# Performance work log

Measured on AMD Instinct MI355X. Metric: run time of the kernel, lower is better.

Reference implementation:

```python
import jax, jax.numpy as jnp
import numpy as np

N_STATE = 1024
N_HEAD = 16
D_K = N_STATE // N_HEAD  # 64


def setup_inputs() -> dict:
    key = jax.random.key(0)
    ks = jax.random.split(key, 12)
    B, S = 2, 2048
    s = 1.0 / np.sqrt(N_STATE)
    inp = {
        "q": jax.random.normal(ks[0], (B, S, N_STATE), jnp.float32),
        "k": jax.random.normal(ks[1], (B, S, N_STATE), jnp.float32),
        "v": jax.random.normal(ks[2], (B, S, N_STATE), jnp.float32),
        # Linear weights in torch layout [out_features, in_features]
        "Wq": jax.random.normal(ks[3], (N_STATE, N_STATE), jnp.float32) * s,
        "bq": jax.random.normal(ks[4], (N_STATE,), jnp.float32) * s,
        "Wk": jax.random.normal(ks[5], (N_STATE, N_STATE), jnp.float32) * s,
        "bk": jax.random.normal(ks[6], (N_STATE,), jnp.float32) * s,
        "Wv": jax.random.normal(ks[7], (N_STATE, N_STATE), jnp.float32) * s,
        "bv": jax.random.normal(ks[8], (N_STATE,), jnp.float32) * s,
        "Wo": jax.random.normal(ks[9], (N_STATE, N_STATE), jnp.float32) * s,
        "bo": jax.random.normal(ks[10], (N_STATE,), jnp.float32) * s,
    }
    return inp


def reference(q, k, v, Wq, bq, Wk, bk, Wv, bv, Wo, bo):
    B = q.shape[0]
    # projections (torch Linear: x @ W.T + b), split heads -> [B, H, S, d]
    def proj(x, W, b):
        y = jnp.einsum('bsi,oi->bso', x, W) + b
        return y.reshape(B, -1, N_HEAD, D_K).transpose(0, 2, 1, 3)
    qh = proj(q, Wq, bq)
    kh = proj(k, Wk, bk)
    vh = proj(v, Wv, bv)
    # scaled dot-product attention, full [B,H,Sq,Sk] scores as in original
    scores = jnp.einsum('bhqd,bhkd->bhqk', qh, kh) / np.sqrt(D_K).astype(np.float32)
    attn = jax.nn.softmax(scores, axis=-1)
    out = jnp.einsum('bhqk,bhkd->bhqd', attn, vh)
    out = out.transpose(0, 2, 1, 3).reshape(B, -1, N_HEAD * D_K)
    return jnp.einsum('bsi,oi->bso', out, Wo) + bo
```

## Files before the change

### kernel.cpp

```cpp
#include <hip/hip_runtime.h>
#include <stdint.h>

typedef __attribute__((ext_vector_type(8))) short short8;
typedef __attribute__((ext_vector_type(4))) float f32x4;
typedef __attribute__((ext_vector_type(4))) uint32_t u32x4;

#if __has_builtin(__builtin_amdgcn_exp2f)
#define EXP2(x) __builtin_amdgcn_exp2f(x)
#else
#define EXP2(x) exp2f(x)
#endif

__device__ __forceinline__ short f2bf(float f){
  uint32_t u = __builtin_bit_cast(uint32_t, f);
  return (short)((u + 0x8000u) >> 16);
}
__device__ __forceinline__ float bf2f(short s){
  return __builtin_bit_cast(float, (uint32_t)(uint16_t)s << 16);
}
__device__ __forceinline__ uint32_t pk2(float lo, float hi){
  uint32_t a = __builtin_bit_cast(uint32_t, lo) + 0x8000u;
  uint32_t b = __builtin_bit_cast(uint32_t, hi) + 0x8000u;
#if __has_builtin(__builtin_amdgcn_perm)
  return __builtin_amdgcn_perm(b, a, 0x07060302u);
#else
  return (b & 0xFFFF0000u) | (a >> 16);
#endif
}
__device__ __forceinline__ void gload16(const void* g, void* l){
  __builtin_amdgcn_global_load_lds((const __attribute__((address_space(1))) void*)g,
                                   (__attribute__((address_space(3))) void*)l, 16, 0, 0);
}

__global__ __launch_bounds__(512) void cvt_all(
    const float* __restrict__ q, const float* __restrict__ k, const float* __restrict__ v,
    const float* __restrict__ wq, const float* __restrict__ wk, const float* __restrict__ wv,
    const float* __restrict__ wo, short* __restrict__ dst){
  const size_t SQ = 4096ull*1024ull, NW = 1024ull*1024ull;
  size_t e = (size_t)(blockIdx.x*512u + threadIdx.x)*8ull;
  const float* src; size_t rel;
  if (e < 3*SQ){ size_t which = e / SQ; src = which==0?q:(which==1?k:v); rel = e - which*SQ; }
  else { size_t e2 = e - 3*SQ; size_t which = e2 / NW;
         src = which==0?wq:(which==1?wk:(which==2?wv:wo)); rel = e2 - which*NW; }
  float4 a = *(const float4*)(src + rel);
  float4 b = *(const float4*)(src + rel + 4);
  u32x4 r = { pk2(a.x,a.y), pk2(a.z,a.w), pk2(b.x,b.y), pk2(b.z,b.w) };
  *(u32x4*)(dst + e) = r;
}

template<int MODE, int NWAVE>
__device__ __forceinline__ void gemm_body(const short* __restrict__ A, const short* __restrict__ Bw,
    const float* __restrict__ bias, void* __restrict__ Cout, float scale, int m0, int n0){
  const int K = 1024;
  const int NT  = NWAVE*64;
  const int SW  = 1024/NT;
  const int RPS = NT/8;
  const int NI  = (NWAVE==4) ? 4 : 2;
  const int WCOL = NI*16;
  __shared__ short Al[128*64];
  __shared__ short Bl[128*64];
  int tid = threadIdx.x;
  int w = tid >> 6, lane = tid & 63, lr = lane & 15, lg = lane >> 4;
  int wr = (NWAVE==4) ? (w >> 1) : (w >> 2);
  int wc = (NWAVE==4) ? (w & 1)  : (w & 3);
  f32x4 acc[4][NI] = {};
  int row0 = tid >> 3;
  int qc0  = (tid & 7) ^ (row0 & 7);
  const short* Ag = A  + (size_t)(m0 + row0)*K + qc0*8;
  const short* Bg = Bw + (size_t)(n0 + row0)*K + qc0*8;
  char* Alb = (char*)Al + tid*16;
  char* Blb = (char*)Bl + tid*16;
  int ra[4], rb[NI];
#pragma unroll
  for (int mi=0; mi<4; ++mi) ra[mi] = wr*64 + mi*16 + lr;
#pragma unroll
  for (int ni=0; ni<NI; ++ni) rb[ni] = wc*WCOL + ni*16 + lr;
  for (int k0 = 0; k0 < K; k0 += 64){
#pragma unroll
    for (int s=0; s<SW; ++s) gload16(Ag + k0 + (size_t)(s*RPS)*K, Alb + s*NT*16);
#pragma unroll
    for (int s=0; s<SW; ++s) gload16(Bg + k0 + (size_t)(s*RPS)*K, Blb + s*NT*16);
    __syncthreads();
#pragma unroll
    for (int kk=0; kk<2; ++kk){
      short8 av[4], bv[NI];
#pragma unroll
      for (int mi=0; mi<4; ++mi)
        av[mi] = *(const short8*)((char*)Al + ra[mi]*128 + (((kk*4 + lg) ^ (ra[mi] & 7)) << 4));
#pragma unroll
      for (int ni=0; ni<NI; ++ni)
        bv[ni] = *(const short8*)((char*)Bl + rb[ni]*128 + (((kk*4 + lg) ^ (rb[ni] & 7)) << 4));
#pragma unroll
      for (int mi=0; mi<4; ++mi)
#pragma unroll
        for (int ni=0; ni<NI; ++ni){
          if (MODE == 2)
            acc[mi][ni] = __builtin_amdgcn_mfma_f32_16x16x32_bf16(bv[ni], av[mi], acc[mi][ni], 0, 0, 0);
          else
            acc[mi][ni] = __builtin_amdgcn_mfma_f32_16x16x32_bf16(av[mi], bv[ni], acc[mi][ni], 0, 0, 0);
        }
    }
    __syncthreads();
  }
#pragma unroll
  for (int ni=0; ni<NI; ++ni){
#pragma unroll
    for (int mi=0; mi<4; ++mi){
      if (MODE == 2){
        int srow = m0 + wr*64 + mi*16 + lr;
        int b = srow >> 11, s = srow & 2047;
#pragma unroll
        for (int i2=0; i2<4; ++i2){
          int dcol = n0 + wc*WCOL + ni*16 + lg*4 + i2;
          int h = dcol >> 6, d = dcol & 63;
          float val = acc[mi][ni][i2] + bias[dcol];
          ((short*)Cout)[(((size_t)(b*16 + h))*64 + d)*2048 + s] = f2bf(val);
        }
      } else {
        int col = n0 + wc*WCOL + ni*16 + lr;
        float bb = bias[col];
#pragma unroll
        for (int i2=0; i2<4; ++i2){
          int row = m0 + wr*64 + mi*16 + lg*4 + i2;
          float val = (acc[mi][ni][i2] + bb) * scale;
          if (MODE == 0){
            int b = row >> 11, s = row & 2047, h = col >> 6, d = col & 63;
            ((short*)Cout)[(((size_t)(b*16 + h))*2048 + s)*64 + d] = f2bf(val);
          } else {
            ((float*)Cout)[(size_t)row*1024 + col] = val;
          }
        }
      }
    }
  }
}

__global__ __launch_bounds__(512) void gemm_qkv(
    const short* __restrict__ qb, const short* __restrict__ kb, const short* __restrict__ vb,
    const short* __restrict__ Wqb, const short* __restrict__ Wkb, const short* __restrict__ Wvb,
    const float* __restrict__ bq, const float* __restrict__ bk, const float* __restrict__ bv,
    short* __restrict__ Qh, short* __restrict__ Kh, short* __restrict__ VhT, float qscale){
  int f = blockIdx.y*gridDim.x + blockIdx.x;
  int L = (f & 7)*96 + (f >> 3);
  int z = L >> 8, r = L & 255;
  int m0 = (r >> 3)*128, n0 = (r & 7)*128;
  const short* A  = z==0 ? qb  : (z==1 ? kb  : vb);
  const short* Bw = z==0 ? Wqb : (z==1 ? Wkb : Wvb);
  const float* bi = z==0 ? bq  : (z==1 ? bk  : bv);
  short* C        = z==0 ? Qh  : (z==1 ? Kh  : VhT);
  if (z == 2) gemm_body<2,8>(A, Bw, bi, (void*)C, 1.0f, m0, n0);
  else        gemm_body<0,8>(A, Bw, bi, (void*)C, z==0 ? qscale : 1.0f, m0, n0);
}

__global__ __launch_bounds__(512) void gemm_out(const short* __restrict__ A, const short* __restrict__ Bw,
    const float* __restrict__ bias, float* __restrict__ Cout){
  int f = blockIdx.y*gridDim.x + blockIdx.x;
  int L = (f & 7)*32 + (f >> 3);
  int m0 = (L >> 3)*128, n0 = (L & 7)*128;
  gemm_body<1,8>(A, Bw, bias, (void*)Cout, 1.0f, m0, n0);
}

__global__ __launch_bounds__(512, 4) void attn_fwd(const short* __restrict__ Qh, const short* __restrict__ Kh,
    const short* __restrict__ VhT, short* __restrict__ Op0, short* __restrict__ Op1,
    float* __restrict__ Ls){
  const int S = 2048;
  int i = blockIdx.y*gridDim.x + blockIdx.x;
  int L = (i & 7)*64 + (i >> 3);
  int bh = L >> 4, r4 = L & 15;
  int qt = r4 >> 1, kh = r4 & 1;
  __shared__ short Kl[4][4096];
  __shared__ short Vl[4][4096];
  int tid = threadIdx.x, w = tid >> 6, lane = tid & 63, lr = lane & 15, lg = lane >> 4;
  const short* Qb = Qh  + (size_t)bh*S*64;
  const short* Kb = Kh  + (size_t)bh*S*64 + (size_t)kh*16*4096;
  const short* Vb = VhT + (size_t)bh*64*2048 + (size_t)kh*16*64;
  short* Op = kh ? Op1 : Op0;
  int q0 = qt*256 + w*32;
  short8 aq[2][2];
#pragma unroll
  for (int m=0; m<2; ++m)
#pragma unroll
    for (int h=0; h<2; ++h)
      aq[m][h] = *(const short8*)&Qb[(size_t)(q0 + m*16 + lr)*64 + h*32 + lg*8];
  f32x4 o[2][4] = {};
  f32x4 o1[2] = {};
  short8 ones;
#pragma unroll
  for (int j=0; j<8; ++j) ones[j] = (short)0x3F80;
  int koff = tid*16;
  int kr = tid >> 3, kc = tid & 7;
  int ksw = (kr & 3) | (((kr >> 3) & 1) << 2);
  int ksrc = kr*64 + ((kc ^ ksw) << 3);
  int vsrc = kr*2048 + ((kc ^ (kr & 7)) << 3);
  int Rbase = 8*(lr >> 2) + (lr & 3);
  int sR = (lr & 3) | (((lr >> 2) & 1) << 2);
  int slot0 = (lg ^ sR) << 3, slot1 = ((lg + 4) ^ sR) << 3;
  int vx = lr & 7;
#pragma unroll
  for (int t=0; t<4; ++t){
    gload16(Kb + (size_t)t*4096 + ksrc, (char*)&Kl[t][0] + koff);
    gload16(Vb + vsrc + t*64,           (char*)&Vl[t][0] + koff);
  }
  asm volatile("s_waitcnt vmcnt(4)" ::: "memory");
  __builtin_amdgcn_sched_barrier(0);
  __builtin_amdgcn_s_barrier();

  for (int p = 0; p < 8; ++p){
    __builtin_amdgcn_s_setprio(1);
#pragma unroll
    for (int u = 0; u < 2; ++u){
      int buf = (2*p + u) & 3;
      const short* Kbuf = &Kl[buf][0];
      short8 pa[2][2];
      {
        uint32_t Wp[2][2][2][2];
#pragma unroll
        for (int nf=0; nf<4; ++nf){
          int R = Rbase + (nf & 1)*4 + (nf >> 1)*32;
          short8 ak0 = *(const short8*)&Kbuf[R*64 + slot0];
          short8 ak1 = *(const short8*)&Kbuf[R*64 + slot1];
#pragma unroll
          for (int m=0; m<2; ++m){
            f32x4 z = {};
            z = __builtin_amdgcn_mfma_f32_16x16x32_bf16(ak0, aq[m][0], z, 0, 0, 0);
            z = __builtin_amdgcn_mfma_f32_16x16x32_bf16(ak1, aq[m][1], z, 0, 0, 0);
            float p0 = EXP2(z[0]), p1 = EXP2(z[1]);
            float p2 = EXP2(z[2]), p3 = EXP2(z[3]);
            Wp[m][nf >> 1][nf & 1][0] = pk2(p0, p1);
            Wp[m][nf >> 1][nf & 1][1] = pk2(p2, p3);
          }
        }
#pragma unroll
        for (int m=0; m<2; ++m)
#pragma unroll
          for (int c=0; c<2; ++c){
            union { uint32_t u4[4]; short8 s; } tt;
            tt.u4[0] = Wp[m][c][0][0]; tt.u4[1] = Wp[m][c][0][1];
            tt.u4[2] = Wp[m][c][1][0]; tt.u4[3] = Wp[m][c][1][1];
            pa[m][c] = tt.s;
          }
      }
      const short* Vbuf = &Vl[buf][0];
#pragma unroll
      for (int df=0; df<4; ++df){
        int rowv = (df*16 + lr)*64;
        short8 vb0 = *(const short8*)&Vbuf[rowv + ((lg ^ vx) << 3)];
        short8 vb1 = *(const short8*)&Vbuf[rowv + (((4 + lg) ^ vx) << 3)];
#pragma unroll
        for (int m=0; m<2; ++m){
          o[m][df] = __builtin_amdgcn_mfma_f32_16x16x32_bf16(pa[m][0], vb0, o[m][df], 0, 0, 0);
          o[m][df] = __builtin_amdgcn_mfma_f32_16x16x32_bf16(pa[m][1], vb1, o[m][df], 0, 0, 0);
        }
      }
#pragma unroll
      for (int m=0; m<2; ++m){
        o1[m] = __builtin_amdgcn_mfma_f32_16x16x32_bf16(pa[m][0], ones, o1[m], 0, 0, 0);
        o1[m] = __builtin_amdgcn_mfma_f32_16x16x32_bf16(pa[m][1], ones, o1[m], 0, 0, 0);
      }
    }
    __builtin_amdgcn_s_setprio(0);
    if (p < 7){
      asm volatile("s_waitcnt vmcnt(0)" ::: "memory");
      __builtin_amdgcn_sched_barrier(0);
      __builtin_amdgcn_s_barrier();
      if (p < 6){
#pragma unroll
        for (int u = 0; u < 2; ++u){
          int t = 2*p + 4 + u, nb = t & 3;
          gload16(Kb + (size_t)t*4096 + ksrc, (char*)&Kl[nb][0] + koff);
          gload16(Vb + vsrc + t*64,           (char*)&Vl[nb][0] + koff);
        }
      }
    }
  }
#pragma unroll
  for (int m=0; m<2; ++m){
#pragma unroll
    for (int df=0; df<4; ++df)
#pragma unroll
      for (int i2=0; i2<4; ++i2){
        int row = q0 + m*16 + lg*4 + i2;
        Op[((size_t)(bh*2048 + row))*64 + df*16 + lr] = f2bf(o[m][df][i2]);
      }
    if (lr == 0){
#pragma unroll
      for (int i2=0; i2<4; ++i2){
        int row = q0 + m*16 + lg*4 + i2;
        Ls[kh*65536 + bh*2048 + row] = o1[m][i2];
      }
    }
  }
}

__global__ __launch_bounds__(256) void attn_merge(const short* __restrict__ Op0, const short* __restrict__ Op1,
    const float* __restrict__ Ls, short* __restrict__ AO){
  size_t e = (size_t)(blockIdx.x*256u + threadIdx.x)*8ull;
  int d = (int)(e & 63);
  size_t rowg = e >> 6;
  float rinv = 1.0f / (Ls[rowg] + Ls[65536 + rowg]);
  short8 a = *(const short8*)&Op0[e];
  short8 b8 = *(const short8*)&Op1[e];
  int bh = (int)(rowg >> 11), qq = (int)(rowg & 2047);
  int b = bh >> 4, h = bh & 15;
  short8 r;
#pragma unroll
  for (int j=0; j<8; ++j) r[j] = f2bf((bf2f(a[j]) + bf2f(b8[j])) * rinv);
  *(short8*)&AO[((size_t)(b*2048 + qq))*1024 + h*64 + d] = r;
}

extern "C" void kernel_launch(void* const* d_in, const int* in_sizes, int n_in,
                              void* d_out, int out_size, void* d_ws, size_t ws_size,
                              hipStream_t stream){
  const float* q  = (const float*)d_in[0];
  const float* k  = (const float*)d_in[1];
  const float* v  = (const float*)d_in[2];
  const float* Wq = (const float*)d_in[3];
  const float* bq = (const float*)d_in[4];
  const float* Wk = (const float*)d_in[5];
  const float* bk = (const float*)d_in[6];
  const float* Wv = (const float*)d_in[7];
  const float* bv = (const float*)d_in[8];
  const float* Wo = (const float*)d_in[9];
  const float* bo = (const float*)d_in[10];

  const size_t SQ = 4096ull*1024ull, NW = 1024ull*1024ull;
  short* ws  = (short*)d_ws;
  short* qb  = ws;
  short* kb  = ws + SQ;
  short* vb  = ws + 2*SQ;
  short* Wqb = ws + 3*SQ;
  short* Wkb = Wqb + NW;
  short* Wvb = Wkb + NW;
  short* Wob = Wvb + NW;
  short* Qh  = Wob + NW;
  short* Kh  = Qh + SQ;
  short* VhT = Kh + SQ;
  short* AO  = qb;
  short* Op0 = kb;
  short* Op1 = vb;
  float* Ls  = (float*)Wqb;

  const float Csc = 0.18033688011112042f;

  cvt_all<<<4096, 512, 0, stream>>>(q, k, v, Wq, Wk, Wv, Wo, ws);
  gemm_qkv<<<dim3(16, 48), 512, 0, stream>>>(qb, kb, vb, Wqb, Wkb, Wvb, bq, bk, bv, Qh, Kh, VhT, Csc);
  attn_fwd<<<dim3(16, 32), 512, 0, stream>>>(Qh, Kh, VhT, Op0, Op1, Ls);
  attn_merge<<<2048, 256, 0, stream>>>(Op0, Op1, Ls, AO);
  gemm_out<<<dim3(16, 16), 512, 0, stream>>>(AO, Wob, bo, (float*)d_out);
}
```

Baseline: 117.1 us.

## Fuse attention split-merge into output projection GEMM A-tile loading

Removes the separate attn_merge kernel. The output-projection GEMM now builds its A tiles on the fly: it reads both partial attention outputs and their row sums, normalises with a fast reciprocal, packs to bf16 and writes the result to shared memory. This saves one launch and a write-then-read round trip of the merged activation through global memory. In exchange, the A loads become synchronous register loads instead of direct-to-LDS loads. Each partial row is also reread by all eight column tiles, which adds L2 traffic and may stall the GEMM main loop.

Result: no change. 119.3 us (+1.9%).

```diff
diff --git a/kernel.cpp b/kernel.cpp
--- a/kernel.cpp
+++ b/kernel.cpp
@@ -9,6 +9,11 @@
 #define EXP2(x) __builtin_amdgcn_exp2f(x)
 #else
 #define EXP2(x) exp2f(x)
+#endif
+#if __has_builtin(__builtin_amdgcn_rcpf)
+#define RCP(x) __builtin_amdgcn_rcpf(x)
+#else
+#define RCP(x) (1.0f/(x))
 #endif
 
 __device__ __forceinline__ short f2bf(float f){
@@ -50,7 +55,8 @@
 
 template<int MODE, int NWAVE>
 __device__ __forceinline__ void gemm_body(const short* __restrict__ A, const short* __restrict__ Bw,
-    const float* __restrict__ bias, void* __restrict__ Cout, float scale, int m0, int n0){
+    const float* __restrict__ bias, void* __restrict__ Cout, float scale, int m0, int n0,
+    const short* __restrict__ P1 = nullptr, const float* __restrict__ Ls = nullptr){
   const int K = 1024;
   const int NT  = NWAVE*64;
   const int SW  = 1024/NT;
@@ -76,8 +82,25 @@
 #pragma unroll
   for (int ni=0; ni<NI; ++ni) rb[ni] = wc*WCOL + ni*16 + lr;
   for (int k0 = 0; k0 < K; k0 += 64){
-#pragma unroll
-    for (int s=0; s<SW; ++s) gload16(Ag + k0 + (size_t)(s*RPS)*K, Alb + s*NT*16);
+    if (MODE == 3){
+      int h = k0 >> 6, d = qc0*8;
+#pragma unroll
+      for (int s=0; s<SW; ++s){
+        int row = m0 + row0 + s*RPS;
+        size_t rg = ((size_t)(((row >> 11) << 4) + h))*2048 + (row & 2047);
+        short8 a0 = *(const short8*)&A [rg*64 + d];
+        short8 a1 = *(const short8*)&P1[rg*64 + d];
+        float rin = RCP(Ls[rg] + Ls[65536 + rg]);
+        float f[8];
+#pragma unroll
+        for (int j=0; j<8; ++j) f[j] = (bf2f(a0[j]) + bf2f(a1[j])) * rin;
+        u32x4 pkv = { pk2(f[0],f[1]), pk2(f[2],f[3]), pk2(f[4],f[5]), pk2(f[6],f[7]) };
+        *(u32x4*)(Alb + s*NT*16) = pkv;
+      }
+    } else {
+#pragma unroll
+      for (int s=0; s<SW; ++s) gload16(Ag + k0 + (size_t)(s*RPS)*K, Alb + s*NT*16);
+    }
 #pragma unroll
     for (int s=0; s<SW; ++s) gload16(Bg + k0 + (size_t)(s*RPS)*K, Blb + s*NT*16);
     __syncthreads();
@@ -152,12 +175,13 @@
   else        gemm_body<0,8>(A, Bw, bi, (void*)C, z==0 ? qscale : 1.0f, m0, n0);
 }
 
-__global__ __launch_bounds__(512) void gemm_out(const short* __restrict__ A, const short* __restrict__ Bw,
+__global__ __launch_bounds__(512) void gemm_out(const short* __restrict__ Op0, const short* __restrict__ Op1,
+    const float* __restrict__ Ls, const short* __restrict__ Bw,
     const float* __restrict__ bias, float* __restrict__ Cout){
   int f = blockIdx.y*gridDim.x + blockIdx.x;
   int L = (f & 7)*32 + (f >> 3);
   int m0 = (L >> 3)*128, n0 = (L & 7)*128;
-  gemm_body<1,8>(A, Bw, bias, (void*)Cout, 1.0f, m0, n0);
+  gemm_body<3,8>(Op0, Bw, bias, (void*)Cout, 1.0f, m0, n0, Op1, Ls);
 }
 
 __global__ __launch_bounds__(512, 4) void attn_fwd(const short* __restrict__ Qh, const short* __restrict__ Kh,
@@ -292,22 +316,6 @@
   }
 }
 
-__global__ __launch_bounds__(256) void attn_merge(const short* __restrict__ Op0, const short* __restrict__ Op1,
-    const float* __restrict__ Ls, short* __restrict__ AO){
-  size_t e = (size_t)(blockIdx.x*256u + threadIdx.x)*8ull;
-  int d = (int)(e & 63);
-  size_t rowg = e >> 6;
-  float rinv = 1.0f / (Ls[rowg] + Ls[65536 + rowg]);
-  short8 a = *(const short8*)&Op0[e];
-  short8 b8 = *(const short8*)&Op1[e];
-  int bh = (int)(rowg >> 11), qq = (int)(rowg & 2047);
-  int b = bh >> 4, h = bh & 15;
-  short8 r;
-#pragma unroll
-  for (int j=0; j<8; ++j) r[j] = f2bf((bf2f(a[j]) + bf2f(b8[j])) * rinv);
-  *(short8*)&AO[((size_t)(b*2048 + qq))*1024 + h*64 + d] = r;
-}
-
 extern "C" void kernel_launch(void* const* d_in, const int* in_sizes, int n_in,
                               void* d_out, int out_size, void* d_ws, size_t ws_size,
                               hipStream_t stream){
@@ -335,7 +343,6 @@
   short* Qh  = Wob + NW;
   short* Kh  = Qh + SQ;
   short* VhT = Kh + SQ;
-  short* AO  = qb;
   short* Op0 = kb;
   short* Op1 = vb;
   float* Ls  = (float*)Wqb;
@@ -345,6 +352,5 @@
   cvt_all<<<4096, 512, 0, stream>>>(q, k, v, Wq, Wk, Wv, Wo, ws);
   gemm_qkv<<<dim3(16, 48), 512, 0, stream>>>(qb, kb, vb, Wqb, Wkb, Wvb, bq, bk, bv, Qh, Kh, VhT, Csc);
   attn_fwd<<<dim3(16, 32), 512, 0, stream>>>(Qh, Kh, VhT, Op0, Op1, Ls);
-  attn_merge<<<2048, 256, 0, stream>>>(Op0, Op1, Ls, AO);
-  gemm_out<<<dim3(16, 16), 512, 0, stream>>>(AO, Wob, bo, (float*)d_out);
-}
+  gemm_out<<<dim3(16, 16), 512, 0, stream>>>(Op0, Op1, Ls, Wob, bo, (float*)d_out);
+}
```
